# Performance work log

Measured on AMD Instinct MI355X. Metric: run time of the kernel, lower is better.

## Reference

```python
import jax, jax.numpy as jnp
import numpy as np

L, H, R, N, E = 6, 128, 64, 10000, 160000
SSILU_SCALE = 1.0 / 0.6  # ScaledSiLU
INV_SQRT_3 = 1.0 / np.sqrt(3.0)
INV_SQRT_H = 1.0 / np.sqrt(H)
INV_SQRT_2 = 1.0 / np.sqrt(2.0)


def ssilu(x):
    return jax.nn.silu(x) * SSILU_SCALE


def lnorm(x, w, b):
    m = x.mean(-1, keepdims=True)
    v = jnp.var(x, axis=-1, keepdims=True)
    return (x - m) * jax.lax.rsqrt(v + 1e-5) * w + b


def gated_block(x, v, wv1, wv2, wu1, bu1, wu2, bu2, hout):
    # GatedEquivariantBlock: x [N,Hin], v [N,3,Hin]
    vec1 = jnp.linalg.norm(jnp.einsum('nci,io->nco', v, wv1), axis=-2)  # [N,Hin]
    vec2 = jnp.einsum('nci,io->nco', v, wv2)                            # [N,3,hout]
    h = ssilu(jnp.concatenate([x, vec1], -1) @ wu1 + bu1) @ wu2 + bu2   # [N,2*hout]
    xs, xv = h[..., :hout], h[..., hout:]
    return ssilu(xs), xv[:, None, :] * vec2


def forward_impl(edge_index, x, vec, edge_rbf, edge_vector,
                 ln_w, ln_b, xp1_w, xp1_b, xp2_w, xp2_b, rbf_w, rbf_b,
                 vp_w, xv1_w, xv1_b, xv2_w, xv2_b,
                 we1, be1, we2, be2,
                 g1_v1, g1_v2, g1_u1, g1_u1b, g1_u2, g1_u2b,
                 g2_v1, g2_v2, g2_u1, g2_u1b, g2_u2, g2_u2b):
    src, dst = edge_index[0], edge_index[1]  # message flows src(j) -> dst(i)
    for l in range(L):
        # ---- PaiNNMessage ----
        xh = ssilu(lnorm(x, ln_w[l], ln_b[l]) @ xp1_w[l] + xp1_b[l]) @ xp2_w[l] + xp2_b[l]  # [N,3H]
        rbfh = edge_rbf @ rbf_w[l] + rbf_b[l]                                                # [E,3H]
        m = xh[src] * rbfh                                                                    # gather + elementwise
        mx = m[:, :H]
        m2 = m[:, H:2 * H] * INV_SQRT_3
        m3 = m[:, 2 * H:]
        mvec = (vec[src] * m2[:, None, :] + m3[:, None, :] * edge_vector[:, :, None]) * INV_SQRT_H  # [E,3,H]
        dx = jax.ops.segment_sum(mx, dst, num_segments=N)
        dvec = jax.ops.segment_sum(mvec, dst, num_segments=N)
        x = (x + dx) * INV_SQRT_2
        vec = vec + dvec
        # ---- PaiNNUpdate ----
        vp = jnp.einsum('nci,io->nco', vec, vp_w[l])  # [N,3,2H]
        v1, v2 = vp[..., :H], vp[..., H:]
        vec_dot = (v1 * v2).sum(axis=1) * INV_SQRT_H  # [N,H]
        vnorm = jnp.sqrt((v2 ** 2).sum(axis=-2) + 1e-8)
        h = ssilu(jnp.concatenate([x, vnorm], -1) @ xv1_w[l] + xv1_b[l]) @ xv2_w[l] + xv2_b[l]  # [N,3H]
        xu1, xu2, xu3 = h[:, :H], h[:, H:2 * H], h[:, 2 * H:]
        x = x + (xu1 + xu2 * vec_dot) * INV_SQRT_2
        vec = vec + xu3[:, None, :] * v1
        # ScaleFactor is identity without a scale file
    energy = ssilu(x @ we1 + be1) @ we2 + be2  # [N,1] per-atom energy
    fx, fv = gated_block(x, vec, g1_v1, g1_v2, g1_u1, g1_u1b, g1_u2, g1_u2b, H // 2)
    fx, fv = gated_block(fx, fv, g2_v1, g2_v2, g2_u1, g2_u1b, g2_u2, g2_u2b, 1)
    forces = fv[..., 0]  # [N,3]
    return jnp.concatenate([energy, forces], axis=-1)  # [N,4] packed (energy, fx, fy, fz)


def setup_inputs() -> dict:
    key = jax.random.key(0)
    ks = iter(jax.random.split(key, 64))
    nrm = lambda shape, s=0.05: jax.random.normal(next(ks), shape, jnp.float32) * s
    return dict(
        x=jax.random.normal(next(ks), (N, H), jnp.float32),
        vec=jax.random.normal(next(ks), (N, 3, H), jnp.float32),
        edge_index=jax.random.randint(next(ks), (2, E), 0, N),
        edge_rbf=jax.random.uniform(next(ks), (E, R), jnp.float32),
        edge_vector=jax.random.normal(next(ks), (E, 3), jnp.float32),
        ln_w=jnp.ones((L, H)), ln_b=jnp.zeros((L, H)),
        xp1_w=nrm((L, H, H)), xp1_b=jnp.zeros((L, H)),
        xp2_w=nrm((L, H, 3 * H)), xp2_b=jnp.zeros((L, 3 * H)),
        rbf_w=nrm((L, R, 3 * H)), rbf_b=jnp.zeros((L, 3 * H)),
        vp_w=nrm((L, H, 2 * H)),
        xv1_w=nrm((L, 2 * H, H)), xv1_b=jnp.zeros((L, H)),
        xv2_w=nrm((L, H, 3 * H)), xv2_b=jnp.zeros((L, 3 * H)),
        we1=nrm((H, H // 2)), be1=jnp.zeros((H // 2,)),
        we2=nrm((H // 2, 1)), be2=jnp.zeros((1,)),
        g1_v1=nrm((H, H)), g1_v2=nrm((H, H // 2)),
        g1_u1=nrm((2 * H, H)), g1_u1b=jnp.zeros((H,)),
        g1_u2=nrm((H, H)), g1_u2b=jnp.zeros((H,)),
        g2_v1=nrm((H // 2, H // 2)), g2_v2=nrm((H // 2, 1)),
        g2_u1=nrm((H, H // 2)), g2_u1b=jnp.zeros((H // 2,)),
        g2_u2=nrm((H // 2, 2)), g2_u2b=jnp.zeros((2,)),
    )


def reference(x, vec, edge_index, edge_rbf, edge_vector,
              ln_w, ln_b, xp1_w, xp1_b, xp2_w, xp2_b, rbf_w, rbf_b,
              vp_w, xv1_w, xv1_b, xv2_w, xv2_b,
              we1, be1, we2, be2,
              g1_v1, g1_v2, g1_u1, g1_u1b, g1_u2, g1_u2b,
              g2_v1, g2_v2, g2_u1, g2_u1b, g2_u2, g2_u2b):
    return forward_impl(edge_index, x, vec, edge_rbf, edge_vector,
                        ln_w, ln_b, xp1_w, xp1_b, xp2_w, xp2_b, rbf_w, rbf_b,
                        vp_w, xv1_w, xv1_b, xv2_w, xv2_b,
                        we1, be1, we2, be2,
                        g1_v1, g1_v2, g1_u1, g1_u1b, g1_u2, g1_u2b,
                        g2_v1, g2_v2, g2_u1, g2_u1b, g2_u2, g2_u2b)
```

## Files before the change

### kernel.cpp

```cpp
#include <hip/hip_runtime.h>
#include <hip/hip_bf16.h>

#define NN 10000
#define EE 160000
#define LL 6

#define INV_SQRT_3f  0.57735026919f
#define INV_SQRT_Hf  0.08838834764832f
#define INV_SQRT_2f  0.70710678118655f

typedef _Float16 half8 __attribute__((ext_vector_type(8)));
typedef float f32x4 __attribute__((ext_vector_type(4)));

#define WE1OFF   0
#define WV1OFF   8192
#define WV2OFF   24576
#define WU1OFF   32768
#define WU2OFF   65536
#define G2V1OFF  81920
#define G2U1OFF  86016
#define WFIN_SZ  94208

__device__ __forceinline__ float ssilu_f(float v){
  float s = 1.0f / (1.0f + __expf(-v));
  return v * s * 1.6666666666667f;
}
__device__ __forceinline__ float bcast(float v, int l){
  return __int_as_float(__builtin_amdgcn_readlane(__float_as_int(v), l));
}

__global__ __launch_bounds__(256) void k_hist(const int* __restrict__ edst, int* __restrict__ cnt){
  int i = blockIdx.x*256 + threadIdx.x;
  if (i < EE) atomicAdd(&cnt[edst[i]], 1);
}

__global__ __launch_bounds__(1024) void k_scan(const int* __restrict__ cnt,
                                               int* __restrict__ off, int* __restrict__ cur){
  __shared__ int ps[1024];
  int t = threadIdx.x;
  int base = t*10;
  int local[10];
  int s = 0;
  #pragma unroll
  for (int i=0;i<10;i++){
    int c = (base+i < NN) ? cnt[base+i] : 0;
    local[i] = s; s += c;
  }
  ps[t] = s;
  __syncthreads();
  for (int d=1; d<1024; d<<=1){
    int v = (t>=d) ? ps[t-d] : 0;
    __syncthreads();
    ps[t] += v;
    __syncthreads();
  }
  int pre = (t>0) ? ps[t-1] : 0;
  #pragma unroll
  for (int i=0;i<10;i++){
    int idx = base+i;
    if (idx < NN){ int o = pre + local[i]; off[idx]=o; cur[idx]=o; }
  }
  if (t==1023) off[NN] = ps[1023];
}

__global__ __launch_bounds__(256) void k_fill(const int* __restrict__ edst,
                                              int* __restrict__ cur, int* __restrict__ eord){
  int i = blockIdx.x*256 + threadIdx.x;
  if (i < EE){
    int d = edst[i];
    int p = atomicAdd(&cur[d], 1);
    eord[p] = i;
  }
}

__global__ __launch_bounds__(256) void k_sorta(const float* __restrict__ erbf,
                                               const int* __restrict__ eord, _Float16* __restrict__ eA){
  long i = (long)blockIdx.x*256 + threadIdx.x;
  if (i >= (long)EE*64) return;
  int j = i & 7, lane = (i >> 3) & 63, kh = (i >> 9) & 1;
  long tile = i >> 10;
  int e = eord[tile*16 + (lane&15)];
  eA[i] = (_Float16)erbf[(size_t)e*64 + kh*32 + (lane>>4)*8 + j];
}

__global__ __launch_bounds__(256) void k_sorte(const int* __restrict__ esrc, const float* __restrict__ evec,
                                               const int* __restrict__ eord, float4* __restrict__ es4){
  int p = blockIdx.x*256 + threadIdx.x;
  if (p >= EE) return;
  int e = eord[p];
  es4[p] = make_float4(evec[(size_t)e*3], evec[(size_t)e*3+1], evec[(size_t)e*3+2],
                       __int_as_float(esrc[e]));
}

__global__ __launch_bounds__(256) void k_packw(const float* __restrict__ w, _Float16* __restrict__ wf){
  int i = blockIdx.x*256 + threadIdx.x;
  if (i >= LL*24*2*64*8) return;
  int j    = i & 7;
  int lane = (i >> 3) & 63;
  int kh   = (i >> 9) & 1;
  int rest = i >> 10;
  int nb   = rest % 24;
  int l    = rest / 24;
  int k    = 32*kh + 8*(lane>>4) + j;
  int ch   = nb*16 + (lane&15);
  float v = w[((size_t)l*64 + k)*384 + ch];
  if (ch >= 128 && ch < 256) v *= INV_SQRT_3f;
  wf[i] = (_Float16)v;
}

__global__ __launch_bounds__(256) void k_packb(const float* __restrict__ b, float* __restrict__ bsc){
  int i = blockIdx.x*256 + threadIdx.x;
  if (i >= LL*384) return;
  int ch = i % 384;
  float v = b[i];
  if (ch >= 128 && ch < 256) v *= INV_SQRT_3f;
  bsc[i] = v;
}

struct PackTab {
  const float* s[40];
  _Float16* d[40];
  int K[40];
  int NO[40];
};
__global__ __launch_bounds__(256) void k_packall(PackTab tb){
  int e = blockIdx.y;
  int K = tb.K[e], NO = tb.NO[e];
  int tot = K*NO, KS = K >> 5;
  const float* s = tb.s[e];
  _Float16* d = tb.d[e];
  for (int i = blockIdx.x*256 + threadIdx.x; i < tot; i += gridDim.x*256){
    int j = i & 7, lane = (i >> 3) & 63, rest = i >> 9;
    int ks = rest % KS, nb = rest / KS;
    int k = ks*32 + (lane>>4)*8 + j, n = nb*16 + (lane&15);
    d[i] = (_Float16)s[(size_t)k*NO + n];
  }
}

__global__ __launch_bounds__(256) void k_cvt16(const float* __restrict__ v, _Float16* __restrict__ o, int n){
  int i = blockIdx.x*256 + threadIdx.x;
  if (i < n) o[i] = (_Float16)v[i];
}

__global__ __launch_bounds__(64) void k_gemm_rbfh(
    const _Float16* __restrict__ eA, const _Float16* __restrict__ wf,
    const float* __restrict__ bsc,
    _Float16* __restrict__ rbfh)
{
  int lane = threadIdx.x;
  int i0 = blockIdx.x * 64;
  int tg = blockIdx.x * 4;
  int ml = lane & 15, kg = lane >> 4;
  half8 a0[4], a1[4];
  #pragma unroll
  for (int tt = 0; tt < 4; tt++){
    a0[tt] = *(const half8*)(eA + ((size_t)((tg+tt)*2+0)*64 + lane)*8);
    a1[tt] = *(const half8*)(eA + ((size_t)((tg+tt)*2+1)*64 + lane)*8);
  }
  #pragma unroll 2
  for (int nb = 0; nb < 24; nb++){
    half8 b0 = *(const half8*)(wf + ((size_t)(nb*2+0)*64 + lane)*8);
    half8 b1 = *(const half8*)(wf + ((size_t)(nb*2+1)*64 + lane)*8);
    float bias = bsc[nb*16 + ml];
    #pragma unroll
    for (int tt = 0; tt < 4; tt++){
      f32x4 acc = {bias, bias, bias, bias};
      acc = __builtin_amdgcn_mfma_f32_16x16x32_f16(a0[tt], b0, acc, 0, 0, 0);
      acc = __builtin_amdgcn_mfma_f32_16x16x32_f16(a1[tt], b1, acc, 0, 0, 0);
      _Float16* orow = rbfh + (size_t)(i0 + tt*16)*384 + nb*16 + ml;
      #pragma unroll
      for (int r = 0; r < 4; r++)
        orow[(size_t)(kg*4 + r)*384] = (_Float16)acc[r];
    }
  }
}

__global__ __launch_bounds__(256) void k_xh_mfma(
    const float* __restrict__ x,
    const float* __restrict__ lnw, const float* __restrict__ lnb,
    const _Float16* __restrict__ wf1, const float* __restrict__ b1,
    const _Float16* __restrict__ wf2, const float* __restrict__ b2,
    _Float16* __restrict__ xh16)
{
  __shared__ _Float16 sA[32][136];
  __shared__ _Float16 sH[32][136];
  int t = threadIdx.x;
  int n0 = blockIdx.x * 32;
  {
    int nd = t >> 3, sb = t & 7;
    int node = n0 + nd;
    float v[16];
    float s = 0.f, ss = 0.f;
    if (node < NN){
      const float* xr = x + (size_t)node*128 + sb*16;
      #pragma unroll
      for (int g = 0; g < 4; g++){
        float4 q = *(const float4*)(xr + g*4);
        v[g*4+0]=q.x; v[g*4+1]=q.y; v[g*4+2]=q.z; v[g*4+3]=q.w;
      }
      #pragma unroll
      for (int u = 0; u < 16; u++){ s += v[u]; ss += v[u]*v[u]; }
    } else {
      #pragma unroll
      for (int u = 0; u < 16; u++) v[u] = 0.f;
    }
    #pragma unroll
    for (int o2 = 4; o2 > 0; o2 >>= 1){
      s  += __shfl_xor(s, o2, 8);
      ss += __shfl_xor(ss, o2, 8);
    }
    float mean = s * (1.0f/128.0f);
    float var  = ss * (1.0f/128.0f) - mean*mean;
    float rstd = rsqrtf(var + 1e-5f);
    #pragma unroll
    for (int u = 0; u < 16; u++){
      int h = sb*16 + u;
      sA[nd][h] = (node < NN) ? (_Float16)((v[u]-mean)*rstd*lnw[h] + lnb[h]) : (_Float16)0.f;
    }
  }
  __syncthreads();
  int lane = t & 63, w = t >> 6, ml = lane & 15, kg = lane >> 4;
  int mt = w >> 1;
  {
    half8 a[4];
    #pragma unroll
    for (int ks = 0; ks < 4; ks++)
      a[ks] = *(const half8*)&sA[mt*16 + ml][ks*32 + kg*8];
    float hout[4][4];
    #pragma unroll
    for (int nb4 = 0; nb4 < 4; nb4++){
      int nb = (w&1)*4 + nb4;
      float bias = b1[nb*16 + ml];
      f32x4 acc = {bias, bias, bias, bias};
      #pragma unroll
      for (int ks = 0; ks < 4; ks++)
        acc = __builtin_amdgcn_mfma_f32_16x16x32_f16(a[ks],
                *(const half8*)(wf1 + ((size_t)(nb*4+ks)*64 + lane)*8), acc, 0,0,0);
      #pragma unroll
      for (int r = 0; r < 4; r++) hout[nb4][r] = ssilu_f(acc[r]);
    }
    #pragma unroll
    for (int nb4 = 0; nb4 < 4; nb4++){
      int nb = (w&1)*4 + nb4;
      #pragma unroll
      for (int r = 0; r < 4; r++)
        sH[mt*16 + kg*4 + r][nb*16 + ml] = (_Float16)hout[nb4][r];
    }
  }
  __syncthreads();
  {
    half8 a[4];
    #pragma unroll
    for (int ks = 0; ks < 4; ks++)
      a[ks] = *(const half8*)&sH[mt*16 + ml][ks*32 + kg*8];
    #pragma unroll 4
    for (int nb12 = 0; nb12 < 12; nb12++){
      int nb = (w&1)*12 + nb12;
      float bias = b2[nb*16 + ml];
      f32x4 acc = {bias, bias, bias, bias};
      #pragma unroll
      for (int ks = 0; ks < 4; ks++)
        acc = __builtin_amdgcn_mfma_f32_16x16x32_f16(a[ks],
                *(const half8*)(wf2 + ((size_t)(nb*4+ks)*64 + lane)*8), acc, 0,0,0);
      #pragma unroll
      for (int r = 0; r < 4; r++){
        int m = mt*16 + kg*4 + r;
        int node = n0 + m;
        if (node < NN) xh16[(size_t)node*384 + nb*16 + ml] = (_Float16)acc[r];
      }
    }
  }
}

__global__ __launch_bounds__(256) void k_edge3(
    const _Float16* __restrict__ rbfh,
    const float4* __restrict__ es4, const int* __restrict__ off,
    const _Float16* __restrict__ xh16, const _Float16* __restrict__ vec16,
    float* __restrict__ dx, float* __restrict__ dvec)
{
  int t = threadIdx.x;
  int lane = t & 63;
  int n = blockIdx.x*4 + (t>>6);
  if (n >= NN) return;
  int o0 = off[n], o1 = off[n+1];
  float ax0 = 0.f, ax1 = 0.f;
  float av00=0.f, av01=0.f, av10=0.f, av11=0.f, av20=0.f, av21=0.f;
  #pragma unroll 2
  for (int p = o0; p < o1; p++){
    const _Float16* hr = rbfh + (size_t)p*384;
    float h0 = (float)hr[lane];
    float h1 = (float)hr[64+lane];
    float h2 = (float)hr[128+lane];
    float h3 = (float)hr[192+lane];
    float h4 = (float)hr[256+lane];
    float h5 = (float)hr[320+lane];
    float4 q = es4[p];
    int sN = __float_as_int(q.w);
    const _Float16* xr = xh16 + (size_t)sN*384;
    float m0  = h0 * (float)xr[lane];
    float m1  = h1 * (float)xr[64+lane];
    float m2a = h2 * (float)xr[128+lane];
    float m2b = h3 * (float)xr[192+lane];
    float m3a = h4 * (float)xr[256+lane];
    float m3b = h5 * (float)xr[320+lane];
    ax0 += m0; ax1 += m1;
    const _Float16* vr = vec16 + (size_t)sN*384;
    av00 = fmaf((float)vr[lane],     m2a, av00); av00 = fmaf(m3a, q.x, av00);
    av01 = fmaf((float)vr[64+lane],  m2b, av01); av01 = fmaf(m3b, q.x, av01);
    av10 = fmaf((float)vr[128+lane], m2a, av10); av10 = fmaf(m3a, q.y, av10);
    av11 = fmaf((float)vr[192+lane], m2b, av11); av11 = fmaf(m3b, q.y, av11);
    av20 = fmaf((float)vr[256+lane], m2a, av20); av20 = fmaf(m3a, q.z, av20);
    av21 = fmaf((float)vr[320+lane], m2b, av21); av21 = fmaf(m3b, q.z, av21);
  }
  float* dxr = dx + (size_t)n*128;
  dxr[lane] = ax0; dxr[64+lane] = ax1;
  float* dvr = dvec + (size_t)n*384;
  dvr[lane]     = av00 * INV_SQRT_Hf;
  dvr[64+lane]  = av01 * INV_SQRT_Hf;
  dvr[128+lane] = av10 * INV_SQRT_Hf;
  dvr[192+lane] = av11 * INV_SQRT_Hf;
  dvr[256+lane] = av20 * INV_SQRT_Hf;
  dvr[320+lane] = av21 * INV_SQRT_Hf;
}

__global__ __launch_bounds__(256) void k_node_mfma(
    float* __restrict__ xbuf, float* __restrict__ vbuf,
    const float* __restrict__ dx, const float* __restrict__ dvec,
    const _Float16* __restrict__ wfvp,
    const _Float16* __restrict__ wfxv1, const float* __restrict__ xv1_b,
    const _Float16* __restrict__ wfxv2, const float* __restrict__ xv2_b,
    _Float16* __restrict__ vec16)
{
  __shared__ _Float16 sV1[96][136];
  __shared__ _Float16 sCat[32][264];
  __shared__ _Float16 sVD[32][128];
  int t = threadIdx.x;
  int n0 = blockIdx.x * 32;
  int lane = t & 63, w = t >> 6, ml = lane & 15, kg = lane >> 4;
  int mt = w & 1, nbb = (w >> 1) * 4;
  float vd[4][4], vn[4][4];
  #pragma unroll
  for (int i=0;i<4;i++){
    #pragma unroll
    for (int r=0;r<4;r++){ vd[i][r]=0.f; vn[i][r]=0.f; }
  }
  int arow = n0 + mt*16 + ml;
  bool aok = arow < NN;
  for (int cd = 0; cd < 3; cd++){
    half8 a[4];
    #pragma unroll
    for (int ks = 0; ks < 4; ks++){
      if (aok){
        const float* vr = vbuf + (size_t)arow*384 + cd*128 + ks*32 + kg*8;
        const float* dr = dvec + (size_t)arow*384 + cd*128 + ks*32 + kg*8;
        float4 q0 = *(const float4*)(vr);
        float4 q1 = *(const float4*)(vr+4);
        float4 d0 = *(const float4*)(dr);
        float4 d1 = *(const float4*)(dr+4);
        a[ks][0]=(_Float16)(q0.x+d0.x); a[ks][1]=(_Float16)(q0.y+d0.y);
        a[ks][2]=(_Float16)(q0.z+d0.z); a[ks][3]=(_Float16)(q0.w+d0.w);
        a[ks][4]=(_Float16)(q1.x+d1.x); a[ks][5]=(_Float16)(q1.y+d1.y);
        a[ks][6]=(_Float16)(q1.z+d1.z); a[ks][7]=(_Float16)(q1.w+d1.w);
      } else {
        #pragma unroll
        for (int j=0;j<8;j++) a[ks][j] = (_Float16)0.f;
      }
    }
    #pragma unroll
    for (int nb4 = 0; nb4 < 4; nb4++){
      int nb1 = nbb + nb4;
      f32x4 acc1 = {0.f,0.f,0.f,0.f}, acc2 = {0.f,0.f,0.f,0.f};
      #pragma unroll
      for (int ks = 0; ks < 4; ks++){
        acc1 = __builtin_amdgcn_mfma_f32_16x16x32_f16(a[ks],
                 *(const half8*)(wfvp + ((size_t)(nb1*4+ks)*64 + lane)*8), acc1, 0,0,0);
// ... 367 lines not shown
                              hipStream_t stream)
{
  const float* x_in   = (const float*)d_in[0];
  const float* vec_in = (const float*)d_in[1];
  const int*   eidx   = (const int*)d_in[2];
  const float* erbf   = (const float*)d_in[3];
  const float* evec   = (const float*)d_in[4];
  const float* ln_w  = (const float*)d_in[5];
  const float* ln_b  = (const float*)d_in[6];
  const float* xp1_w = (const float*)d_in[7];
  const float* xp1_b = (const float*)d_in[8];
  const float* xp2_w = (const float*)d_in[9];
  const float* xp2_b = (const float*)d_in[10];
  const float* rbf_w = (const float*)d_in[11];
  const float* rbf_b = (const float*)d_in[12];
  const float* vp_w  = (const float*)d_in[13];
  const float* xv1_w = (const float*)d_in[14];
  const float* xv1_b = (const float*)d_in[15];
  const float* xv2_w = (const float*)d_in[16];
  const float* xv2_b = (const float*)d_in[17];
  const float* we1 = (const float*)d_in[18];
  const float* be1 = (const float*)d_in[19];
  const float* we2 = (const float*)d_in[20];
  const float* be2 = (const float*)d_in[21];
  const float* g1_v1 = (const float*)d_in[22];
  const float* g1_v2 = (const float*)d_in[23];
  const float* g1_u1 = (const float*)d_in[24];
  const float* g1_u1b = (const float*)d_in[25];
  const float* g1_u2 = (const float*)d_in[26];
  const float* g1_u2b = (const float*)d_in[27];
  const float* g2_v1 = (const float*)d_in[28];
  const float* g2_v2 = (const float*)d_in[29];
  const float* g2_u1 = (const float*)d_in[30];
  const float* g2_u1b = (const float*)d_in[31];
  const float* g2_u2 = (const float*)d_in[32];
  const float* g2_u2b = (const float*)d_in[33];
  float* out = (float*)d_out;

  char* base = (char*)d_ws;
  size_t o = 0;
  auto alloc = [&](size_t bytes) -> char* {
    char* p = base + o;
    o = (o + bytes + 255) & ~(size_t)255;
    return p;
  };
  float* x_cur   = (float*)alloc((size_t)NN*128*4);
  float* vec_cur = (float*)alloc((size_t)NN*384*4);
  float* dx      = (float*)alloc((size_t)NN*128*4);
  float* dvec    = (float*)alloc((size_t)NN*384*4);
  _Float16* xh16 = (_Float16*)alloc((size_t)NN*384*2);
  _Float16* vec16= (_Float16*)alloc((size_t)NN*384*2);
  int*   eord    = (int*)alloc((size_t)EE*4);
  int*   off     = (int*)alloc((size_t)(NN+1)*4);
  _Float16* wf   = (_Float16*)alloc((size_t)LL*24576*2);
  float* bsc     = (float*)alloc((size_t)LL*384*4);
  _Float16* wfn  = (_Float16*)alloc((size_t)LL*180224*2);
  _Float16* wfin = (_Float16*)alloc((size_t)WFIN_SZ*2);
  _Float16* eA   = (_Float16*)alloc((size_t)EE*64*2);
  float4* es4    = (float4*)alloc((size_t)EE*16);
  _Float16* rbfh = (_Float16*)alloc((size_t)EE*384*2);
  int* cnt = (int*)dx;
  int* cur = cnt + NN;

  hipMemcpyAsync(x_cur, x_in, sizeof(float)*(size_t)NN*128, hipMemcpyDeviceToDevice, stream);
  hipMemcpyAsync(vec_cur, vec_in, sizeof(float)*(size_t)NN*384, hipMemcpyDeviceToDevice, stream);

  const int* esrc = eidx;
  const int* edst = eidx + EE;

  hipMemsetAsync(cnt, 0, sizeof(int)*NN, stream);
  k_hist<<<(EE+255)/256, 256, 0, stream>>>(edst, cnt);
  k_scan<<<1, 1024, 0, stream>>>(cnt, off, cur);
  k_fill<<<(EE+255)/256, 256, 0, stream>>>(edst, cur, eord);
  k_sorta<<<(EE*64+255)/256, 256, 0, stream>>>(erbf, eord, eA);
  k_sorte<<<(EE+255)/256, 256, 0, stream>>>(esrc, evec, eord, es4);
  k_packw<<<(LL*24576+255)/256, 256, 0, stream>>>(rbf_w, wf);
  k_packb<<<(LL*384+255)/256, 256, 0, stream>>>(rbf_b, bsc);
  k_cvt16<<<(NN*384+255)/256, 256, 0, stream>>>(vec_in, vec16, NN*384);

  {
    PackTab tb;
    for (int l = 0; l < LL; l++){
      _Float16* wb = wfn + (size_t)l*180224;
      tb.s[l*5+0] = xp1_w + (size_t)l*128*128; tb.d[l*5+0] = wb;          tb.K[l*5+0]=128; tb.NO[l*5+0]=128;
      tb.s[l*5+1] = xp2_w + (size_t)l*128*384; tb.d[l*5+1] = wb+16384;    tb.K[l*5+1]=128; tb.NO[l*5+1]=384;
      tb.s[l*5+2] = vp_w  + (size_t)l*128*256; tb.d[l*5+2] = wb+65536;    tb.K[l*5+2]=128; tb.NO[l*5+2]=256;
      tb.s[l*5+3] = xv1_w + (size_t)l*256*128; tb.d[l*5+3] = wb+98304;    tb.K[l*5+3]=256; tb.NO[l*5+3]=128;
      tb.s[l*5+4] = xv2_w + (size_t)l*128*384; tb.d[l*5+4] = wb+131072;   tb.K[l*5+4]=128; tb.NO[l*5+4]=384;
    }
    tb.s[30] = we1;   tb.d[30] = wfin + WE1OFF;  tb.K[30]=128; tb.NO[30]=64;
    tb.s[31] = g1_v1; tb.d[31] = wfin + WV1OFF;  tb.K[31]=128; tb.NO[31]=128;
    tb.s[32] = g1_v2; tb.d[32] = wfin + WV2OFF;  tb.K[32]=128; tb.NO[32]=64;
    tb.s[33] = g1_u1; tb.d[33] = wfin + WU1OFF;  tb.K[33]=256; tb.NO[33]=128;
    tb.s[34] = g1_u2; tb.d[34] = wfin + WU2OFF;  tb.K[34]=128; tb.NO[34]=128;
    tb.s[35] = g2_v1; tb.d[35] = wfin + G2V1OFF; tb.K[35]=64;  tb.NO[35]=64;
    tb.s[36] = g2_u1; tb.d[36] = wfin + G2U1OFF; tb.K[36]=128; tb.NO[36]=64;
    k_packall<<<dim3(24, 37), 256, 0, stream>>>(tb);
  }

  for (int l = 0; l < LL; l++){
    _Float16* wb = wfn + (size_t)l*180224;
    k_xh_mfma<<<(NN+31)/32, 256, 0, stream>>>(x_cur, ln_w + l*128, ln_b + l*128,
        wb, xp1_b + l*128, wb+16384, xp2_b + l*384, xh16);
    k_gemm_rbfh<<<EE/64, 64, 0, stream>>>(eA, wf + (size_t)l*24576,
        bsc + (size_t)l*384, rbfh);
    k_edge3<<<NN/4, 256, 0, stream>>>(rbfh, es4, off, xh16, vec16, dx, dvec);
    k_node_mfma<<<(NN+31)/32, 256, 0, stream>>>(x_cur, vec_cur, dx, dvec,
        wb+65536, wb+98304, xv1_b + l*128, wb+131072, xv2_b + l*384, vec16);
  }
  k_final<<<(NN+31)/32, 256, 0, stream>>>(x_cur, vec_cur, wfin,
      be1, we2, be2, g1_u1b, g1_u2b, g2_v2, g2_u1b, g2_u2, g2_u2b, out);
}
```

Baseline: 972.6 us.

## Fuse RBF projection GEMM into edge message aggregation kernel

Merges the per-edge rbf GEMM and the edge gather/aggregation into one kernel. Each block handles 8 destination nodes, computes 16-edge rbfh tiles with MFMA into shared memory, then accumulates messages into shared-memory per-node accumulators via LDS atomics. This removes the EE×384 fp16 rbfh intermediate write and re-read from global memory. In exchange it adds LDS atomics, per-tile segment-boundary logic, and recomputes boundary tiles shared between blocks.

```diff
diff --git a/kernel.cpp b/kernel.cpp
--- a/kernel.cpp
+++ b/kernel.cpp
@@ -142,36 +142,96 @@
   if (i < n) o[i] = (_Float16)v[i];
 }
 
-__global__ __launch_bounds__(64) void k_gemm_rbfh(
+__global__ __launch_bounds__(256) void k_edge_fused(
     const _Float16* __restrict__ eA, const _Float16* __restrict__ wf,
     const float* __restrict__ bsc,
-    _Float16* __restrict__ rbfh)
+    const float4* __restrict__ es4, const int* __restrict__ off,
+    const _Float16* __restrict__ xh16, const _Float16* __restrict__ vec16,
+    float* __restrict__ dx, float* __restrict__ dvec)
 {
-  int lane = threadIdx.x;
-  int i0 = blockIdx.x * 64;
-  int tg = blockIdx.x * 4;
-  int ml = lane & 15, kg = lane >> 4;
-  half8 a0[4], a1[4];
-  #pragma unroll
-  for (int tt = 0; tt < 4; tt++){
-    a0[tt] = *(const half8*)(eA + ((size_t)((tg+tt)*2+0)*64 + lane)*8);
-    a1[tt] = *(const half8*)(eA + ((size_t)((tg+tt)*2+1)*64 + lane)*8);
-  }
-  #pragma unroll 2
-  for (int nb = 0; nb < 24; nb++){
-    half8 b0 = *(const half8*)(wf + ((size_t)(nb*2+0)*64 + lane)*8);
-    half8 b1 = *(const half8*)(wf + ((size_t)(nb*2+1)*64 + lane)*8);
-    float bias = bsc[nb*16 + ml];
-    #pragma unroll
-    for (int tt = 0; tt < 4; tt++){
-      f32x4 acc = {bias, bias, bias, bias};
-      acc = __builtin_amdgcn_mfma_f32_16x16x32_f16(a0[tt], b0, acc, 0, 0, 0);
-      acc = __builtin_amdgcn_mfma_f32_16x16x32_f16(a1[tt], b1, acc, 0, 0, 0);
-      _Float16* orow = rbfh + (size_t)(i0 + tt*16)*384 + nb*16 + ml;
-      #pragma unroll
-      for (int r = 0; r < 4; r++)
-        orow[(size_t)(kg*4 + r)*384] = (_Float16)acc[r];
-    }
+  __shared__ _Float16 sT[4][16][204];
+  __shared__ float dxacc[8][128];
+  __shared__ float dvacc[8][384];
+  __shared__ int s_off[9];
+  int t = threadIdx.x;
+  int n0 = blockIdx.x * 8;
+  {
+    float* pz = &dxacc[0][0];
+    for (int i = t; i < 8*128; i += 256) pz[i] = 0.f;
+    float* qz = &dvacc[0][0];
+    for (int i = t; i < 8*384; i += 256) qz[i] = 0.f;
+    if (t < 9) s_off[t] = off[n0 + t];
+  }
+  __syncthreads();
+  int lane = t & 63, w = t >> 6, ml = lane & 15, kg = lane >> 4;
+  int o0 = s_off[0], o8 = s_off[8];
+  int T0 = o0 >> 4;
+  int T1 = (o8 - 1) >> 4;
+  for (int tile = T0 + w; tile <= T1; tile += 4){
+    half8 a0 = *(const half8*)(eA + ((size_t)(tile*2+0)*64 + lane)*8);
+    half8 a1 = *(const half8*)(eA + ((size_t)(tile*2+1)*64 + lane)*8);
+    int pstart = max(tile*16, o0), pend = min(tile*16+16, o8);
+    #pragma unroll
+    for (int hf = 0; hf < 2; hf++){
+      #pragma unroll
+      for (int g = 0; g < 3; g++){
+        #pragma unroll
+        for (int q = 0; q < 4; q++){
+          int nb = g*8 + hf*4 + q;
+          float bias = bsc[nb*16 + ml];
+          f32x4 acc = {bias, bias, bias, bias};
+          acc = __builtin_amdgcn_mfma_f32_16x16x32_f16(a0,
+                  *(const half8*)(wf + ((size_t)(nb*2+0)*64 + lane)*8), acc, 0,0,0);
+          acc = __builtin_amdgcn_mfma_f32_16x16x32_f16(a1,
+                  *(const half8*)(wf + ((size_t)(nb*2+1)*64 + lane)*8), acc, 0,0,0);
+          #pragma unroll
+          for (int r = 0; r < 4; r++)
+            sT[w][kg*4 + r][g*64 + q*16 + ml] = (_Float16)acc[r];
+        }
+      }
+      int c = 0;
+      while (c < 7 && pstart >= s_off[c+1]) c++;
+      int hofs = hf*64;
+      float ax = 0.f, av0 = 0.f, av1 = 0.f, av2 = 0.f;
+      for (int p = pstart; p < pend; p++){
+        if (p >= s_off[c+1]){
+          atomicAdd(&dxacc[c][hofs + lane], ax);
+          atomicAdd(&dvacc[c][hofs + lane], av0);
+          atomicAdd(&dvacc[c][128 + hofs + lane], av1);
+          atomicAdd(&dvacc[c][256 + hofs + lane], av2);
+          ax = 0.f; av0 = 0.f; av1 = 0.f; av2 = 0.f;
+          do { c++; } while (c < 7 && p >= s_off[c+1]);
+        }
+        int e = p - tile*16;
+        float hm  = (float)sT[w][e][lane];
+        float hm2 = (float)sT[w][e][64 + lane];
+        float hm3 = (float)sT[w][e][128 + lane];
+        float4 q4 = es4[p];
+        int sN = __float_as_int(q4.w);
+        const _Float16* xr = xh16 + (size_t)sN*384 + hofs;
+        float m0 = hm  * (float)xr[lane];
+        float m2 = hm2 * (float)xr[128 + lane];
+        float m3 = hm3 * (float)xr[256 + lane];
+        ax += m0;
+        const _Float16* vr = vec16 + (size_t)sN*384 + hofs;
+        av0 = fmaf((float)vr[lane],       m2, av0); av0 = fmaf(m3, q4.x, av0);
+        av1 = fmaf((float)vr[128 + lane], m2, av1); av1 = fmaf(m3, q4.y, av1);
+        av2 = fmaf((float)vr[256 + lane], m2, av2); av2 = fmaf(m3, q4.z, av2);
+      }
+      atomicAdd(&dxacc[c][hofs + lane], ax);
+      atomicAdd(&dvacc[c][hofs + lane], av0);
+      atomicAdd(&dvacc[c][128 + hofs + lane], av1);
+      atomicAdd(&dvacc[c][256 + hofs + lane], av2);
+    }
+  }
+  __syncthreads();
+  for (int i = t; i < 8*128; i += 256){
+    int nd = i >> 7, hh = i & 127;
+    dx[(size_t)(n0+nd)*128 + hh] = dxacc[nd][hh];
+  }
+  for (int i = t; i < 8*384; i += 256){
+    int nd = i / 384, hh = i % 384;
+    dvec[(size_t)(n0+nd)*384 + hh] = dvacc[nd][hh] * INV_SQRT_Hf;
   }
 }
 
@@ -270,57 +330,6 @@
       }
     }
   }
-}
-
-__global__ __launch_bounds__(256) void k_edge3(
-    const _Float16* __restrict__ rbfh,
-    const float4* __restrict__ es4, const int* __restrict__ off,
-    const _Float16* __restrict__ xh16, const _Float16* __restrict__ vec16,
-    float* __restrict__ dx, float* __restrict__ dvec)
-{
-  int t = threadIdx.x;
-  int lane = t & 63;
-  int n = blockIdx.x*4 + (t>>6);
-  if (n >= NN) return;
-  int o0 = off[n], o1 = off[n+1];
-  float ax0 = 0.f, ax1 = 0.f;
-  float av00=0.f, av01=0.f, av10=0.f, av11=0.f, av20=0.f, av21=0.f;
-  #pragma unroll 2
-  for (int p = o0; p < o1; p++){
-    const _Float16* hr = rbfh + (size_t)p*384;
-    float h0 = (float)hr[lane];
-    float h1 = (float)hr[64+lane];
-    float h2 = (float)hr[128+lane];
-    float h3 = (float)hr[192+lane];
-    float h4 = (float)hr[256+lane];
-    float h5 = (float)hr[320+lane];
-    float4 q = es4[p];
-    int sN = __float_as_int(q.w);
-    const _Float16* xr = xh16 + (size_t)sN*384;
-    float m0  = h0 * (float)xr[lane];
-    float m1  = h1 * (float)xr[64+lane];
-    float m2a = h2 * (float)xr[128+lane];
-    float m2b = h3 * (float)xr[192+lane];
-    float m3a = h4 * (float)xr[256+lane];
-    float m3b = h5 * (float)xr[320+lane];
-    ax0 += m0; ax1 += m1;
-    const _Float16* vr = vec16 + (size_t)sN*384;
-    av00 = fmaf((float)vr[lane],     m2a, av00); av00 = fmaf(m3a, q.x, av00);
-    av01 = fmaf((float)vr[64+lane],  m2b, av01); av01 = fmaf(m3b, q.x, av01);
-    av10 = fmaf((float)vr[128+lane], m2a, av10); av10 = fmaf(m3a, q.y, av10);
-    av11 = fmaf((float)vr[192+lane], m2b, av11); av11 = fmaf(m3b, q.y, av11);
-    av20 = fmaf((float)vr[256+lane], m2a, av20); av20 = fmaf(m3a, q.z, av20);
-    av21 = fmaf((float)vr[320+lane], m2b, av21); av21 = fmaf(m3b, q.z, av21);
-  }
-  float* dxr = dx + (size_t)n*128;
-  dxr[lane] = ax0; dxr[64+lane] = ax1;
-  float* dvr = dvec + (size_t)n*384;
-  dvr[lane]     = av00 * INV_SQRT_Hf;
-  dvr[64+lane]  = av01 * INV_SQRT_Hf;
-  dvr[128+lane] = av10 * INV_SQRT_Hf;
-  dvr[192+lane] = av11 * INV_SQRT_Hf;
-  dvr[256+lane] = av20 * INV_SQRT_Hf;
-  dvr[320+lane] = av21 * INV_SQRT_Hf;
 }
 
 __global__ __launch_bounds__(256) void k_node_mfma(
@@ -800,7 +809,6 @@
   _Float16* wfin = (_Float16*)alloc((size_t)WFIN_SZ*2);
   _Float16* eA   = (_Float16*)alloc((size_t)EE*64*2);
   float4* es4    = (float4*)alloc((size_t)EE*16);
-  _Float16* rbfh = (_Float16*)alloc((size_t)EE*384*2);
   int* cnt = (int*)dx;
   int* cur = cnt + NN;
 
@@ -844,9 +852,8 @@
     _Float16* wb = wfn + (size_t)l*180224;
     k_xh_mfma<<<(NN+31)/32, 256, 0, stream>>>(x_cur, ln_w + l*128, ln_b + l*128,
         wb, xp1_b + l*128, wb+16384, xp2_b + l*384, xh16);
-    k_gemm_rbfh<<<EE/64, 64, 0, stream>>>(eA, wf + (size_t)l*24576,
-        bsc + (size_t)l*384, rbfh);
-    k_edge3<<<NN/4, 256, 0, stream>>>(rbfh, es4, off, xh16, vec16, dx, dvec);
+    k_edge_fused<<<NN/8, 256, 0, stream>>>(eA, wf + (size_t)l*24576,
+        bsc + (size_t)l*384, es4, off, xh16, vec16, dx, dvec);
     k_node_mfma<<<(NN+31)/32, 256, 0, stream>>>(x_cur, vec_cur, dx, dvec,
         wb+65536, wb+98304, xv1_b + l*128, wb+131072, xv2_b + l*384, vec16);
   }
```

Result: slower. 2.157 ms (+121.8%).

## Split edge aggregation per half-feature and schedule nodes by descending degree

Applied to the files above, without the earlier changes.

Adds a one-time counting sort of nodes by in-degree, capped at 63, into descending order. The edge aggregation kernel now gives each wave one half of the 128 features of a node instead of all of it. A persistent grid of 8192 waves walks three strided passes over the sorted list, in serpentine order, to balance work across waves. The aim is to cut load imbalance and tail effects from uneven degree, at the cost of loading the edge metadata twice per edge and fewer accumulators per wave.

```diff
diff --git a/kernel.cpp b/kernel.cpp
--- a/kernel.cpp
+++ b/kernel.cpp
@@ -70,6 +70,25 @@
     int d = edst[i];
     int p = atomicAdd(&cur[d], 1);
     eord[p] = i;
+  }
+}
+
+__global__ __launch_bounds__(256) void k_dhist(const int* __restrict__ cnt, int* __restrict__ dh){
+  int n = blockIdx.x*256 + threadIdx.x;
+  if (n < NN) atomicAdd(&dh[min(cnt[n], 63)], 1);
+}
+__global__ __launch_bounds__(64) void k_dscan(const int* __restrict__ dh, int* __restrict__ dcur){
+  if (threadIdx.x == 0){
+    int acc = 0;
+    for (int d = 63; d >= 0; d--){ dcur[d] = acc; acc += dh[d]; }
+  }
+}
+__global__ __launch_bounds__(256) void k_dscat(const int* __restrict__ cnt,
+                                               int* __restrict__ dcur, int* __restrict__ order){
+  int n = blockIdx.x*256 + threadIdx.x;
+  if (n < NN){
+    int p = atomicAdd(&dcur[min(cnt[n], 63)], 1);
+    order[p] = n;
   }
 }
 
@@ -272,55 +291,49 @@
   }
 }
 
-__global__ __launch_bounds__(256) void k_edge3(
+__global__ __launch_bounds__(256) void k_edge5(
     const _Float16* __restrict__ rbfh,
     const float4* __restrict__ es4, const int* __restrict__ off,
+    const int* __restrict__ order,
     const _Float16* __restrict__ xh16, const _Float16* __restrict__ vec16,
     float* __restrict__ dx, float* __restrict__ dvec)
 {
   int t = threadIdx.x;
   int lane = t & 63;
-  int n = blockIdx.x*4 + (t>>6);
-  if (n >= NN) return;
-  int o0 = off[n], o1 = off[n+1];
-  float ax0 = 0.f, ax1 = 0.f;
-  float av00=0.f, av01=0.f, av10=0.f, av11=0.f, av20=0.f, av21=0.f;
-  #pragma unroll 2
-  for (int p = o0; p < o1; p++){
-    const _Float16* hr = rbfh + (size_t)p*384;
-    float h0 = (float)hr[lane];
-    float h1 = (float)hr[64+lane];
-    float h2 = (float)hr[128+lane];
-    float h3 = (float)hr[192+lane];
-    float h4 = (float)hr[256+lane];
-    float h5 = (float)hr[320+lane];
-    float4 q = es4[p];
-    int sN = __float_as_int(q.w);
-    const _Float16* xr = xh16 + (size_t)sN*384;
-    float m0  = h0 * (float)xr[lane];
-    float m1  = h1 * (float)xr[64+lane];
-    float m2a = h2 * (float)xr[128+lane];
-    float m2b = h3 * (float)xr[192+lane];
-    float m3a = h4 * (float)xr[256+lane];
-    float m3b = h5 * (float)xr[320+lane];
-    ax0 += m0; ax1 += m1;
-    const _Float16* vr = vec16 + (size_t)sN*384;
-    av00 = fmaf((float)vr[lane],     m2a, av00); av00 = fmaf(m3a, q.x, av00);
-    av01 = fmaf((float)vr[64+lane],  m2b, av01); av01 = fmaf(m3b, q.x, av01);
-    av10 = fmaf((float)vr[128+lane], m2a, av10); av10 = fmaf(m3a, q.y, av10);
-    av11 = fmaf((float)vr[192+lane], m2b, av11); av11 = fmaf(m3b, q.y, av11);
-    av20 = fmaf((float)vr[256+lane], m2a, av20); av20 = fmaf(m3a, q.z, av20);
-    av21 = fmaf((float)vr[320+lane], m2b, av21); av21 = fmaf(m3b, q.z, av21);
-  }
-  float* dxr = dx + (size_t)n*128;
-  dxr[lane] = ax0; dxr[64+lane] = ax1;
-  float* dvr = dvec + (size_t)n*384;
-  dvr[lane]     = av00 * INV_SQRT_Hf;
-  dvr[64+lane]  = av01 * INV_SQRT_Hf;
-  dvr[128+lane] = av10 * INV_SQRT_Hf;
-  dvr[192+lane] = av11 * INV_SQRT_Hf;
-  dvr[256+lane] = av20 * INV_SQRT_Hf;
-  dvr[320+lane] = av21 * INV_SQRT_Hf;
+  int wv = blockIdx.x*4 + (t>>6);
+  const int NW = 8192;
+  #pragma unroll 1
+  for (int k = 0; k < 3; k++){
+    int i = k*NW + ((k & 1) ? (NW-1-wv) : wv);
+    if (i >= 2*NN) continue;
+    int n = order[i >> 1];
+    int hofs = (i & 1) * 64;
+    int o0 = off[n], o1 = off[n+1];
+    float ax = 0.f, av0 = 0.f, av1 = 0.f, av2 = 0.f;
+    #pragma unroll 2
+    for (int p = o0; p < o1; p++){
+      const _Float16* hr = rbfh + (size_t)p*384 + hofs;
+      float h0 = (float)hr[lane];
+      float h2 = (float)hr[128+lane];
+      float h3 = (float)hr[256+lane];
+      float4 q = es4[p];
+      int sN = __float_as_int(q.w);
+      const _Float16* xr = xh16 + (size_t)sN*384 + hofs;
+      float m0 = h0 * (float)xr[lane];
+      float m2 = h2 * (float)xr[128+lane];
+      float m3 = h3 * (float)xr[256+lane];
+      ax += m0;
+      const _Float16* vr = vec16 + (size_t)sN*384 + hofs;
+      av0 = fmaf((float)vr[lane],     m2, av0); av0 = fmaf(m3, q.x, av0);
+      av1 = fmaf((float)vr[128+lane], m2, av1); av1 = fmaf(m3, q.y, av1);
+      av2 = fmaf((float)vr[256+lane], m2, av2); av2 = fmaf(m3, q.z, av2);
+    }
+    dx[(size_t)n*128 + hofs + lane] = ax;
+    float* dvr = dvec + (size_t)n*384 + hofs;
+    dvr[lane]     = av0 * INV_SQRT_Hf;
+    dvr[128+lane] = av1 * INV_SQRT_Hf;
+    dvr[256+lane] = av2 * INV_SQRT_Hf;
+  }
 }
 
 __global__ __launch_bounds__(256) void k_node_mfma(
@@ -794,6 +807,9 @@
   _Float16* vec16= (_Float16*)alloc((size_t)NN*384*2);
   int*   eord    = (int*)alloc((size_t)EE*4);
   int*   off     = (int*)alloc((size_t)(NN+1)*4);
+  int*   order   = (int*)alloc((size_t)NN*4);
+  int*   dh      = (int*)alloc(64*4);
+  int*   dcur    = (int*)alloc(64*4);
   _Float16* wf   = (_Float16*)alloc((size_t)LL*24576*2);
   float* bsc     = (float*)alloc((size_t)LL*384*4);
   _Float16* wfn  = (_Float16*)alloc((size_t)LL*180224*2);
@@ -811,9 +827,13 @@
   const int* edst = eidx + EE;
 
   hipMemsetAsync(cnt, 0, sizeof(int)*NN, stream);
+  hipMemsetAsync(dh, 0, sizeof(int)*64, stream);
   k_hist<<<(EE+255)/256, 256, 0, stream>>>(edst, cnt);
   k_scan<<<1, 1024, 0, stream>>>(cnt, off, cur);
   k_fill<<<(EE+255)/256, 256, 0, stream>>>(edst, cur, eord);
+  k_dhist<<<(NN+255)/256, 256, 0, stream>>>(cnt, dh);
+  k_dscan<<<1, 64, 0, stream>>>(dh, dcur);
+  k_dscat<<<(NN+255)/256, 256, 0, stream>>>(cnt, dcur, order);
   k_sorta<<<(EE*64+255)/256, 256, 0, stream>>>(erbf, eord, eA);
   k_sorte<<<(EE+255)/256, 256, 0, stream>>>(esrc, evec, eord, es4);
   k_packw<<<(LL*24576+255)/256, 256, 0, stream>>>(rbf_w, wf);
@@ -846,7 +866,7 @@
         wb, xp1_b + l*128, wb+16384, xp2_b + l*384, xh16);
     k_gemm_rbfh<<<EE/64, 64, 0, stream>>>(eA, wf + (size_t)l*24576,
         bsc + (size_t)l*384, rbfh);
-    k_edge3<<<NN/4, 256, 0, stream>>>(rbfh, es4, off, xh16, vec16, dx, dvec);
+    k_edge5<<<2048, 256, 0, stream>>>(rbfh, es4, off, order, xh16, vec16, dx, dvec);
     k_node_mfma<<<(NN+31)/32, 256, 0, stream>>>(x_cur, vec_cur, dx, dvec,
         wb+65536, wb+98304, xv1_b + l*128, wb+131072, xv2_b + l*384, vec16);
   }
```

After: 1.029 ms. +5.8%, slower.

## Fuse rbf GEMM into edge message kernel with segmented atomic scatter

Applied to the files above, without the earlier changes.

Merges the per-layer rbf projection GEMM with the edge message/aggregation kernel. Each wavefront computes a 16-edge tile's rbfh into shared memory and immediately consumes it, so the E×384 fp16 rbfh buffer is never written to or read back from global memory. Aggregation switches from per-node CSR ownership to per-tile segmented reduction over dst-sorted edges, flushed with atomicAdds, which requires zeroing dx/dvec with memsets each layer. It adds atomic traffic where a node's edges span tiles, and float atomics make the summation order nondeterministic.

```diff
diff --git a/kernel.cpp b/kernel.cpp
--- a/kernel.cpp
+++ b/kernel.cpp
@@ -83,13 +83,16 @@
   eA[i] = (_Float16)erbf[(size_t)e*64 + kh*32 + (lane>>4)*8 + j];
 }
 
-__global__ __launch_bounds__(256) void k_sorte(const int* __restrict__ esrc, const float* __restrict__ evec,
-                                               const int* __restrict__ eord, float4* __restrict__ es4){
+__global__ __launch_bounds__(256) void k_sorte(const int* __restrict__ esrc, const int* __restrict__ edst,
+                                               const float* __restrict__ evec,
+                                               const int* __restrict__ eord, float4* __restrict__ es4,
+                                               int* __restrict__ dord){
   int p = blockIdx.x*256 + threadIdx.x;
   if (p >= EE) return;
   int e = eord[p];
   es4[p] = make_float4(evec[(size_t)e*3], evec[(size_t)e*3+1], evec[(size_t)e*3+2],
                        __int_as_float(esrc[e]));
+  dord[p] = edst[e];
 }
 
 __global__ __launch_bounds__(256) void k_packw(const float* __restrict__ w, _Float16* __restrict__ wf){
@@ -142,158 +145,64 @@
   if (i < n) o[i] = (_Float16)v[i];
 }
 
-__global__ __launch_bounds__(64) void k_gemm_rbfh(
+#define MSTR 388
+__global__ __launch_bounds__(256) void k_edge_mf(
     const _Float16* __restrict__ eA, const _Float16* __restrict__ wf,
     const float* __restrict__ bsc,
-    _Float16* __restrict__ rbfh)
+    const float4* __restrict__ es4, const int* __restrict__ dord,
+    const _Float16* __restrict__ xh16, const _Float16* __restrict__ vec16,
+    float* __restrict__ dx, float* __restrict__ dvec)
 {
-  int lane = threadIdx.x;
-  int i0 = blockIdx.x * 64;
-  int tg = blockIdx.x * 4;
+  __shared__ _Float16 sM[4][16][MSTR];
+  int t = threadIdx.x;
+  int lane = t & 63, w = t >> 6;
+  int tile = blockIdx.x*4 + w;
   int ml = lane & 15, kg = lane >> 4;
-  half8 a0[4], a1[4];
-  #pragma unroll
-  for (int tt = 0; tt < 4; tt++){
-    a0[tt] = *(const half8*)(eA + ((size_t)((tg+tt)*2+0)*64 + lane)*8);
-    a1[tt] = *(const half8*)(eA + ((size_t)((tg+tt)*2+1)*64 + lane)*8);
-  }
+  _Float16* mw = &sM[w][0][0];
+
+  half8 a0 = *(const half8*)(eA + ((size_t)(tile*2+0)*64 + lane)*8);
+  half8 a1 = *(const half8*)(eA + ((size_t)(tile*2+1)*64 + lane)*8);
   #pragma unroll 2
   for (int nb = 0; nb < 24; nb++){
     half8 b0 = *(const half8*)(wf + ((size_t)(nb*2+0)*64 + lane)*8);
     half8 b1 = *(const half8*)(wf + ((size_t)(nb*2+1)*64 + lane)*8);
     float bias = bsc[nb*16 + ml];
-    #pragma unroll
-    for (int tt = 0; tt < 4; tt++){
-      f32x4 acc = {bias, bias, bias, bias};
-      acc = __builtin_amdgcn_mfma_f32_16x16x32_f16(a0[tt], b0, acc, 0, 0, 0);
-      acc = __builtin_amdgcn_mfma_f32_16x16x32_f16(a1[tt], b1, acc, 0, 0, 0);
-      _Float16* orow = rbfh + (size_t)(i0 + tt*16)*384 + nb*16 + ml;
-      #pragma unroll
-      for (int r = 0; r < 4; r++)
-        orow[(size_t)(kg*4 + r)*384] = (_Float16)acc[r];
-    }
-  }
-}
-
-__global__ __launch_bounds__(256) void k_xh_mfma(
-    const float* __restrict__ x,
-    const float* __restrict__ lnw, const float* __restrict__ lnb,
-    const _Float16* __restrict__ wf1, const float* __restrict__ b1,
-    const _Float16* __restrict__ wf2, const float* __restrict__ b2,
-    _Float16* __restrict__ xh16)
-{
-  __shared__ _Float16 sA[32][136];
-  __shared__ _Float16 sH[32][136];
-  int t = threadIdx.x;
-  int n0 = blockIdx.x * 32;
-  {
-    int nd = t >> 3, sb = t & 7;
-    int node = n0 + nd;
-    float v[16];
-    float s = 0.f, ss = 0.f;
-    if (node < NN){
-      const float* xr = x + (size_t)node*128 + sb*16;
-      #pragma unroll
-      for (int g = 0; g < 4; g++){
-        float4 q = *(const float4*)(xr + g*4);
-        v[g*4+0]=q.x; v[g*4+1]=q.y; v[g*4+2]=q.z; v[g*4+3]=q.w;
-      }
-      #pragma unroll
-      for (int u = 0; u < 16; u++){ s += v[u]; ss += v[u]*v[u]; }
-    } else {
-      #pragma unroll
-      for (int u = 0; u < 16; u++) v[u] = 0.f;
-    }
-    #pragma unroll
-    for (int o2 = 4; o2 > 0; o2 >>= 1){
-      s  += __shfl_xor(s, o2, 8);
-      ss += __shfl_xor(ss, o2, 8);
-    }
-    float mean = s * (1.0f/128.0f);
-    float var  = ss * (1.0f/128.0f) - mean*mean;
-    float rstd = rsqrtf(var + 1e-5f);
-    #pragma unroll
-    for (int u = 0; u < 16; u++){
-      int h = sb*16 + u;
-      sA[nd][h] = (node < NN) ? (_Float16)((v[u]-mean)*rstd*lnw[h] + lnb[h]) : (_Float16)0.f;
-    }
-  }
-  __syncthreads();
-  int lane = t & 63, w = t >> 6, ml = lane & 15, kg = lane >> 4;
-  int mt = w >> 1;
-  {
-    half8 a[4];
-    #pragma unroll
-    for (int ks = 0; ks < 4; ks++)
-      a[ks] = *(const half8*)&sA[mt*16 + ml][ks*32 + kg*8];
-    float hout[4][4];
-    #pragma unroll
-    for (int nb4 = 0; nb4 < 4; nb4++){
-      int nb = (w&1)*4 + nb4;
-      float bias = b1[nb*16 + ml];
-      f32x4 acc = {bias, bias, bias, bias};
-      #pragma unroll
-      for (int ks = 0; ks < 4; ks++)
-        acc = __builtin_amdgcn_mfma_f32_16x16x32_f16(a[ks],
-                *(const half8*)(wf1 + ((size_t)(nb*4+ks)*64 + lane)*8), acc, 0,0,0);
-      #pragma unroll
-      for (int r = 0; r < 4; r++) hout[nb4][r] = ssilu_f(acc[r]);
-    }
-    #pragma unroll
-    for (int nb4 = 0; nb4 < 4; nb4++){
-      int nb = (w&1)*4 + nb4;
-      #pragma unroll
-      for (int r = 0; r < 4; r++)
-        sH[mt*16 + kg*4 + r][nb*16 + ml] = (_Float16)hout[nb4][r];
-    }
-  }
-  __syncthreads();
-  {
-    half8 a[4];
-    #pragma unroll
-    for (int ks = 0; ks < 4; ks++)
-      a[ks] = *(const half8*)&sH[mt*16 + ml][ks*32 + kg*8];
-    #pragma unroll 4
-    for (int nb12 = 0; nb12 < 12; nb12++){
-      int nb = (w&1)*12 + nb12;
-      float bias = b2[nb*16 + ml];
-      f32x4 acc = {bias, bias, bias, bias};
-      #pragma unroll
-      for (int ks = 0; ks < 4; ks++)
-        acc = __builtin_amdgcn_mfma_f32_16x16x32_f16(a[ks],
-                *(const half8*)(wf2 + ((size_t)(nb*4+ks)*64 + lane)*8), acc, 0,0,0);
-      #pragma unroll
-      for (int r = 0; r < 4; r++){
-        int m = mt*16 + kg*4 + r;
-        int node = n0 + m;
-        if (node < NN) xh16[(size_t)node*384 + nb*16 + ml] = (_Float16)acc[r];
-      }
-    }
-  }
-}
-
-__global__ __launch_bounds__(256) void k_edge3(
-    const _Float16* __restrict__ rbfh,
-    const float4* __restrict__ es4, const int* __restrict__ off,
-    const _Float16* __restrict__ xh16, const _Float16* __restrict__ vec16,
-    float* __restrict__ dx, float* __restrict__ dvec)
-{
-  int t = threadIdx.x;
-  int lane = t & 63;
-  int n = blockIdx.x*4 + (t>>6);
-  if (n >= NN) return;
-  int o0 = off[n], o1 = off[n+1];
-  float ax0 = 0.f, ax1 = 0.f;
+    f32x4 acc = {bias, bias, bias, bias};
+    acc = __builtin_amdgcn_mfma_f32_16x16x32_f16(a0, b0, acc, 0, 0, 0);
+    acc = __builtin_amdgcn_mfma_f32_16x16x32_f16(a1, b1, acc, 0, 0, 0);
+    #pragma unroll
+    for (int r = 0; r < 4; r++)
+      mw[(kg*4 + r)*MSTR + nb*16 + ml] = (_Float16)acc[r];
+  }
+
+  int p0 = tile*16;
+  float ax0=0.f, ax1=0.f;
   float av00=0.f, av01=0.f, av10=0.f, av11=0.f, av20=0.f, av21=0.f;
-  #pragma unroll 2
-  for (int p = o0; p < o1; p++){
-    const _Float16* hr = rbfh + (size_t)p*384;
-    float h0 = (float)hr[lane];
-    float h1 = (float)hr[64+lane];
-    float h2 = (float)hr[128+lane];
-    float h3 = (float)hr[192+lane];
-    float h4 = (float)hr[256+lane];
-    float h5 = (float)hr[320+lane];
+  int prev = dord[p0];
+  for (int e = 0; e < 16; e++){
+    int p = p0 + e;
+    int d = dord[p];
+    if (d != prev){
+      float* dxr = dx + (size_t)prev*128;
+      atomicAdd(dxr + lane, ax0);
+      atomicAdd(dxr + 64 + lane, ax1);
+      float* dvr = dvec + (size_t)prev*384;
+      atomicAdd(dvr + lane,       av00 * INV_SQRT_Hf);
+      atomicAdd(dvr + 64 + lane,  av01 * INV_SQRT_Hf);
+      atomicAdd(dvr + 128 + lane, av10 * INV_SQRT_Hf);
+      atomicAdd(dvr + 192 + lane, av11 * INV_SQRT_Hf);
+      atomicAdd(dvr + 256 + lane, av20 * INV_SQRT_Hf);
+      atomicAdd(dvr + 320 + lane, av21 * INV_SQRT_Hf);
+      ax0=0.f; ax1=0.f; av00=0.f; av01=0.f; av10=0.f; av11=0.f; av20=0.f; av21=0.f;
+      prev = d;
+    }
+    const _Float16* me = mw + e*MSTR;
+    float h0 = (float)me[lane];
+    float h1 = (float)me[64+lane];
+    float h2 = (float)me[128+lane];
+    float h3 = (float)me[192+lane];
+    float h4 = (float)me[256+lane];
+    float h5 = (float)me[320+lane];
     float4 q = es4[p];
     int sN = __float_as_int(q.w);
     const _Float16* xr = xh16 + (size_t)sN*384;
@@ -312,15 +221,115 @@
     av20 = fmaf((float)vr[256+lane], m2a, av20); av20 = fmaf(m3a, q.z, av20);
     av21 = fmaf((float)vr[320+lane], m2b, av21); av21 = fmaf(m3b, q.z, av21);
   }
-  float* dxr = dx + (size_t)n*128;
-  dxr[lane] = ax0; dxr[64+lane] = ax1;
-  float* dvr = dvec + (size_t)n*384;
-  dvr[lane]     = av00 * INV_SQRT_Hf;
-  dvr[64+lane]  = av01 * INV_SQRT_Hf;
-  dvr[128+lane] = av10 * INV_SQRT_Hf;
-  dvr[192+lane] = av11 * INV_SQRT_Hf;
-  dvr[256+lane] = av20 * INV_SQRT_Hf;
-  dvr[320+lane] = av21 * INV_SQRT_Hf;
+  {
+    float* dxr = dx + (size_t)prev*128;
+    atomicAdd(dxr + lane, ax0);
+    atomicAdd(dxr + 64 + lane, ax1);
+    float* dvr = dvec + (size_t)prev*384;
+    atomicAdd(dvr + lane,       av00 * INV_SQRT_Hf);
+    atomicAdd(dvr + 64 + lane,  av01 * INV_SQRT_Hf);
+    atomicAdd(dvr + 128 + lane, av10 * INV_SQRT_Hf);
+    atomicAdd(dvr + 192 + lane, av11 * INV_SQRT_Hf);
+    atomicAdd(dvr + 256 + lane, av20 * INV_SQRT_Hf);
+    atomicAdd(dvr + 320 + lane, av21 * INV_SQRT_Hf);
+  }
+}
+
+__global__ __launch_bounds__(256) void k_xh_mfma(
+    const float* __restrict__ x,
+    const float* __restrict__ lnw, const float* __restrict__ lnb,
+    const _Float16* __restrict__ wf1, const float* __restrict__ b1,
+    const _Float16* __restrict__ wf2, const float* __restrict__ b2,
+    _Float16* __restrict__ xh16)
+{
+  __shared__ _Float16 sA[32][136];
+  __shared__ _Float16 sH[32][136];
+  int t = threadIdx.x;
+  int n0 = blockIdx.x * 32;
+  {
+    int nd = t >> 3, sb = t & 7;
+    int node = n0 + nd;
+    float v[16];
+    float s = 0.f, ss = 0.f;
+    if (node < NN){
+      const float* xr = x + (size_t)node*128 + sb*16;
+      #pragma unroll
+      for (int g = 0; g < 4; g++){
+        float4 q = *(const float4*)(xr + g*4);
+        v[g*4+0]=q.x; v[g*4+1]=q.y; v[g*4+2]=q.z; v[g*4+3]=q.w;
+      }
+      #pragma unroll
+      for (int u = 0; u < 16; u++){ s += v[u]; ss += v[u]*v[u]; }
+    } else {
+      #pragma unroll
+      for (int u = 0; u < 16; u++) v[u] = 0.f;
+    }
+    #pragma unroll
+    for (int o2 = 4; o2 > 0; o2 >>= 1){
+      s  += __shfl_xor(s, o2, 8);
+      ss += __shfl_xor(ss, o2, 8);
+    }
+    float mean = s * (1.0f/128.0f);
+    float var  = ss * (1.0f/128.0f) - mean*mean;
+    float rstd = rsqrtf(var + 1e-5f);
+    #pragma unroll
+    for (int u = 0; u < 16; u++){
+      int h = sb*16 + u;
+      sA[nd][h] = (node < NN) ? (_Float16)((v[u]-mean)*rstd*lnw[h] + lnb[h]) : (_Float16)0.f;
+    }
+  }
+  __syncthreads();
+  int lane = t & 63, w = t >> 6, ml = lane & 15, kg = lane >> 4;
+  int mt = w >> 1;
+  {
+    half8 a[4];
+    #pragma unroll
+    for (int ks = 0; ks < 4; ks++)
+      a[ks] = *(const half8*)&sA[mt*16 + ml][ks*32 + kg*8];
+    float hout[4][4];
+    #pragma unroll
+    for (int nb4 = 0; nb4 < 4; nb4++){
+      int nb = (w&1)*4 + nb4;
+      float bias = b1[nb*16 + ml];
+      f32x4 acc = {bias, bias, bias, bias};
+      #pragma unroll
+      for (int ks = 0; ks < 4; ks++)
+        acc = __builtin_amdgcn_mfma_f32_16x16x32_f16(a[ks],
+                *(const half8*)(wf1 + ((size_t)(nb*4+ks)*64 + lane)*8), acc, 0,0,0);
+      #pragma unroll
+      for (int r = 0; r < 4; r++) hout[nb4][r] = ssilu_f(acc[r]);
+    }
+    #pragma unroll
+    for (int nb4 = 0; nb4 < 4; nb4++){
+      int nb = (w&1)*4 + nb4;
+      #pragma unroll
+      for (int r = 0; r < 4; r++)
+        sH[mt*16 + kg*4 + r][nb*16 + ml] = (_Float16)hout[nb4][r];
+    }
+  }
+  __syncthreads();
+  {
+    half8 a[4];
+    #pragma unroll
+    for (int ks = 0; ks < 4; ks++)
+      a[ks] = *(const half8*)&sH[mt*16 + ml][ks*32 + kg*8];
+    #pragma unroll 4
+    for (int nb12 = 0; nb12 < 12; nb12++){
+      int nb = (w&1)*12 + nb12;
+      float bias = b2[nb*16 + ml];
+      f32x4 acc = {bias, bias, bias, bias};
+      #pragma unroll
+      for (int ks = 0; ks < 4; ks++)
+        acc = __builtin_amdgcn_mfma_f32_16x16x32_f16(a[ks],
+                *(const half8*)(wf2 + ((size_t)(nb*4+ks)*64 + lane)*8), acc, 0,0,0);
+      #pragma unroll
+      for (int r = 0; r < 4; r++){
+        int m = mt*16 + kg*4 + r;
+        int node = n0 + m;
+        if (node < NN) xh16[(size_t)node*384 + nb*16 + ml] = (_Float16)acc[r];
+      }
+    }
+  }
 }
 
 __global__ __launch_bounds__(256) void k_node_mfma(
@@ -794,13 +803,13 @@
   _Float16* vec16= (_Float16*)alloc((size_t)NN*384*2);
   int*   eord    = (int*)alloc((size_t)EE*4);
   int*   off     = (int*)alloc((size_t)(NN+1)*4);
+  int*   dord    = (int*)alloc((size_t)EE*4);
   _Float16* wf   = (_Float16*)alloc((size_t)LL*24576*2);
   float* bsc     = (float*)alloc((size_t)LL*384*4);
   _Float16* wfn  = (_Float16*)alloc((size_t)LL*180224*2);
   _Float16* wfin = (_Float16*)alloc((size_t)WFIN_SZ*2);
   _Float16* eA   = (_Float16*)alloc((size_t)EE*64*2);
   float4* es4    = (float4*)alloc((size_t)EE*16);
-  _Float16* rbfh = (_Float16*)alloc((size_t)EE*384*2);
   int* cnt = (int*)dx;
   int* cur = cnt + NN;
 
@@ -815,7 +824,7 @@
   k_scan<<<1, 1024, 0, stream>>>(cnt, off, cur);
   k_fill<<<(EE+255)/256, 256, 0, stream>>>(edst, cur, eord);
   k_sorta<<<(EE*64+255)/256, 256, 0, stream>>>(erbf, eord, eA);
-  k_sorte<<<(EE+255)/256, 256, 0, stream>>>(esrc, evec, eord, es4);
+  k_sorte<<<(EE+255)/256, 256, 0, stream>>>(esrc, edst, evec, eord, es4, dord);
   k_packw<<<(LL*24576+255)/256, 256, 0, stream>>>(rbf_w, wf);
   k_packb<<<(LL*384+255)/256, 256, 0, stream>>>(rbf_b, bsc);
   k_cvt16<<<(NN*384+255)/256, 256, 0, stream>>>(vec_in, vec16, NN*384);
@@ -842,11 +851,12 @@
 
   for (int l = 0; l < LL; l++){
     _Float16* wb = wfn + (size_t)l*180224;
+    hipMemsetAsync(dx, 0, sizeof(float)*(size_t)NN*128, stream);
+    hipMemsetAsync(dvec, 0, sizeof(float)*(size_t)NN*384, stream);
     k_xh_mfma<<<(NN+31)/32, 256, 0, stream>>>(x_cur, ln_w + l*128, ln_b + l*128,
         wb, xp1_b + l*128, wb+16384, xp2_b + l*384, xh16);
-    k_gemm_rbfh<<<EE/64, 64, 0, stream>>>(eA, wf + (size_t)l*24576,
-        bsc + (size_t)l*384, rbfh);
-    k_edge3<<<NN/4, 256, 0, stream>>>(rbfh, es4, off, xh16, vec16, dx, dvec);
+    k_edge_mf<<<2500, 256, 0, stream>>>(eA, wf + (size_t)l*24576,
+        bsc + (size_t)l*384, es4, dord, xh16, vec16, dx, dvec);
     k_node_mfma<<<(NN+31)/32, 256, 0, stream>>>(x_cur, vec_cur, dx, dvec,
         wb+65536, wb+98304, xv1_b + l*128, wb+131072, xv2_b + l*384, vec16);
   }
```

After: 1.032 ms. 1.06x slower.
